# Performance work log

Hardware: AMD Instinct MI355X
Metric: run time of the kernel (lower is better)

Reference implementation:

```python
import jax, jax.numpy as jnp
import numpy as np

N_USERS = 60000
N_ITEMS = 40000
N = N_USERS + N_ITEMS   # ncount
EMB = 64
NNZ = 3200000           # nnz of sparse_norm_adj (avg degree 32)
LN_EPS = 1e-5


def setup_inputs() -> dict:
    key = jax.random.key(0)
    ks = jax.random.split(key, 12)
    ego = jax.random.normal(ks[0], (N, EMB), jnp.float32) * 0.1
    rows = jax.random.randint(ks[1], (NNZ,), 0, N)
    cols = jax.random.randint(ks[2], (NNZ,), 0, N)
    # normalized adjacency values (non-trainable buffer)
    vals = jax.random.uniform(ks[3], (NNZ,), jnp.float32) * 0.01
    # xavier-uniform-ish scale for [64,64]: sqrt(2/(64+64)) = 0.125
    w_uu = jax.random.normal(ks[4], (EMB, EMB), jnp.float32) * 0.125
    filt_uu = jax.random.uniform(ks[5], (N_USERS,), jnp.float32, 0.99, 1.01)
    par_uu = jax.random.uniform(ks[6], (2,), jnp.float32, 0.0, 0.99)
    w_ii = jax.random.normal(ks[7], (EMB, EMB), jnp.float32) * 0.125
    filt_ii = jax.random.uniform(ks[8], (N_ITEMS,), jnp.float32, 0.99, 1.01)
    par_ii = jax.random.uniform(ks[9], (2,), jnp.float32, 0.0, 0.99)
    ln_gamma = jnp.ones((EMB,), jnp.float32)
    ln_beta = jnp.zeros((EMB,), jnp.float32)
    return {"ego_embeddings": ego, "rows": rows, "cols": cols, "vals": vals,
            "w_uu": w_uu, "filt_uu": filt_uu, "par_uu": par_uu,
            "w_ii": w_ii, "filt_ii": filt_ii, "par_ii": par_ii,
            "ln_gamma": ln_gamma, "ln_beta": ln_beta}


def _spmm(rows, cols, vals, x):
    # out[rows] += vals * x[cols]  <=>  sparse_adj @ x
    return jax.ops.segment_sum(vals[:, None] * x[cols], rows, num_segments=N)


def reference(ego_embeddings, rows, cols, vals, w_uu, filt_uu, par_uu,
              w_ii, filt_ii, par_ii, ln_gamma, ln_beta):
    res = ego_embeddings
    u = ego_embeddings[:N_USERS]
    it = ego_embeddings[N_USERS:]
    # HWNN layer with K1=K2=1 collapses to par0*par1 * diag(filter) @ X @ W
    user_ego = par_uu[0] * par_uu[1] * ((filt_uu[:, None] * u) @ w_uu) + u
    item_ego = par_ii[0] * par_ii[1] * ((filt_ii[:, None] * it) @ w_ii) + it
    ego = jnp.concatenate([user_ego, item_ego], axis=0)  # [N, EMB]
    # HGCNConv (act=False): adj @ (adj.T @ ego)
    h = jax.ops.segment_sum(vals[:, None] * ego[rows], cols, num_segments=N)  # adj.T @ ego
    y = _spmm(rows, cols, vals, h)                                            # adj @ h
    # LayerNorm (eps=1e-5, affine) + residual from the ORIGINAL input
    mu = jnp.mean(y, axis=-1, keepdims=True)
    var = jnp.var(y, axis=-1, keepdims=True)
    yn = (y - mu) / jnp.sqrt(var + LN_EPS) * ln_gamma + ln_beta
    out = yn + res
    return out[:N_USERS], out[N_USERS:]
```

## Files before the change

### kernel.cpp

```cpp
#include <hip/hip_runtime.h>

#define N_USERS 60000
#define N_ITEMS 40000
#define N_TOTAL 100000
#define EMB 64
#define LN_EPS 1e-5f

#define KPS 128
#define KSH 7
#define NSUP ((N_TOTAL + KPS - 1) / KPS)
#define EPB 4096
#define BLT 512
#define TR_ROWS 32
#define XPITCH 68
#define CAP 2048
#define SPT 512

__device__ __forceinline__ float bf2f(unsigned short h)
{ return __uint_as_float(((unsigned)h) << 16); }
__device__ __forceinline__ unsigned short f2bf(float f)
{
    unsigned u = __float_as_uint(f);
    return (unsigned short)((u + 0x7FFFu + ((u >> 16) & 1u)) >> 16);
}

__global__ void transform_tile(const float* __restrict__ x,
                               const float* __restrict__ w_uu,
                               const float* __restrict__ filt_uu,
                               const float* __restrict__ par_uu,
                               const float* __restrict__ w_ii,
                               const float* __restrict__ filt_ii,
                               const float* __restrict__ par_ii,
                               unsigned short* __restrict__ out)
{
    __shared__ float Wls[EMB * EMB];
    __shared__ float xs[TR_ROWS * XPITCH];
    const int tid = threadIdx.x;
    const int r0 = blockIdx.x * TR_ROWS;
    const int itm = (r0 >= N_USERS);
    const float* W  = itm ? w_ii : w_uu;
    const float* fb = itm ? filt_ii : filt_uu;
    const int foff  = itm ? N_USERS : 0;
    const float c   = itm ? par_ii[0] * par_ii[1] : par_uu[0] * par_uu[1];

    for (int i = tid; i < EMB * EMB / 4; i += 256)
        ((float4*)Wls)[i] = ((const float4*)W)[i];
    for (int i = tid; i < TR_ROWS * 16; i += 256) {
        const float4 v = ((const float4*)x)[r0 * 16 + i];
        *(float4*)&xs[(i >> 4) * XPITCH + (i & 15) * 4] = v;
    }
    __syncthreads();

    const int lane = tid & 63;
    const int wv = tid >> 6;
    const int rg = lane >> 4;
    const int j  = lane & 15;

#pragma unroll
    for (int it = 0; it < 2; ++it) {
        const int rl = wv * 8 + it * 4 + rg;
        const int row = r0 + rl;
        float4 acc = make_float4(0.f, 0.f, 0.f, 0.f);
#pragma unroll 8
        for (int k = 0; k < EMB; ++k) {
            const float xb = xs[rl * XPITCH + k];
            const float4 w4 = *(const float4*)&Wls[k * EMB + 4 * j];
            acc.x += xb * w4.x; acc.y += xb * w4.y;
            acc.z += xb * w4.z; acc.w += xb * w4.w;
        }
        const float cf = c * fb[row - foff];
        const float4 xv = *(const float4*)&xs[rl * XPITCH + 4 * j];
        ushort4 o;
        o.x = f2bf(cf * acc.x + xv.x);
        o.y = f2bf(cf * acc.y + xv.y);
        o.z = f2bf(cf * acc.z + xv.z);
        o.w = f2bf(cf * acc.w + xv.w);
        *(ushort4*)&out[(size_t)row * EMB + 4 * j] = o;
    }
}

__global__ void hist_sup(const int* __restrict__ rows,
                         const int* __restrict__ cols,
                         int* __restrict__ cnt_r,
                         int* __restrict__ cnt_c, int nnz)
{
    __shared__ int hr[NSUP], hc[NSUP];
    const int tid = threadIdx.x;
    for (int i = tid; i < NSUP; i += 256) { hr[i] = 0; hc[i] = 0; }
    __syncthreads();
    for (int e = blockIdx.x * 256 + tid; e < nnz; e += gridDim.x * 256) {
        atomicAdd(&hr[rows[e] >> KSH], 1);
        atomicAdd(&hc[cols[e] >> KSH], 1);
    }
    __syncthreads();
    for (int i = tid; i < NSUP; i += 256) {
        if (hr[i]) atomicAdd(&cnt_r[i], hr[i]);
        if (hc[i]) atomicAdd(&cnt_c[i], hc[i]);
    }
}

__global__ void scan_sup(const int* __restrict__ cnt_c, int* __restrict__ base_c,
                         int* __restrict__ cur_c,
                         const int* __restrict__ cnt_r, int* __restrict__ base_r,
                         int* __restrict__ cur_r)
{
    const int* cnt = blockIdx.x ? cnt_r : cnt_c;
    int* base = blockIdx.x ? base_r : base_c;
    int* cur  = blockIdx.x ? cur_r  : cur_c;
    __shared__ int wsum[16];
    const int i = threadIdx.x;
    const int lane = i & 63;
    const int wv = i >> 6;
    const int v = (i < NSUP) ? cnt[i] : 0;
    int incl = v;
#pragma unroll
    for (int off = 1; off < 64; off <<= 1) {
        const int t = __shfl_up(incl, off, 64);
        if (lane >= off) incl += t;
    }
    if (lane == 63) wsum[wv] = incl;
    __syncthreads();
    if (i == 0) {
        int run = 0;
#pragma unroll
        for (int w = 0; w < 16; ++w) { const int t = wsum[w]; wsum[w] = run; run += t; }
        base[NSUP] = run;
    }
    __syncthreads();
    const int excl = wsum[wv] + incl - v;
    if (i < NSUP) { base[i] = excl; cur[i] = excl; }
}

__global__ void __launch_bounds__(BLT, 3)
build_both(const int* __restrict__ rows,
           const int* __restrict__ cols,
           const float* __restrict__ vals,
           int* __restrict__ cur_c, int2* __restrict__ pairs_c,
           int* __restrict__ cur_r, int2* __restrict__ pairs_r, int nnz)
{
    __shared__ int2 stage[EPB];
    __shared__ unsigned short sg[EPB];
    __shared__ int hist_c[NSUP];
    __shared__ int hist_r[NSUP];
    __shared__ int gbase[NSUP];
    __shared__ int lcur[NSUP];
    __shared__ int wsum[8];

    const int tid = threadIdx.x;
    const int e0 = blockIdx.x * EPB;
    const int ecnt = min(EPB, nnz - e0);

    for (int i = tid; i < NSUP; i += BLT) { hist_c[i] = 0; hist_r[i] = 0; }
    __syncthreads();

    int myr[EPB / BLT], myc[EPB / BLT];
    float myv[EPB / BLT];
#pragma unroll
    for (int i = 0; i < EPB / BLT; ++i) {
        const int s = tid + i * BLT;
        if (s < ecnt) {
            const int e = e0 + s;
            myr[i] = rows[e]; myc[i] = cols[e]; myv[i] = vals[e];
            atomicAdd(&hist_c[myc[i] >> KSH], 1);
            atomicAdd(&hist_r[myr[i] >> KSH], 1);
        } else myr[i] = -1;
    }
    __syncthreads();

#pragma unroll 1
    for (int p = 0; p < 2; ++p) {
        int* hist = p ? hist_r : hist_c;
        int* gcur = p ? cur_r  : cur_c;
        int2* out = p ? pairs_r : pairs_c;

        {
            const int lane = tid & 63;
            const int wv = tid >> 6;
            const int i0 = tid * 2;
            const int va = (i0     < NSUP) ? hist[i0]     : 0;
            const int vb = (i0 + 1 < NSUP) ? hist[i0 + 1] : 0;
            const int tsum = va + vb;
            int incl = tsum;
#pragma unroll
            for (int off = 1; off < 64; off <<= 1) {
                const int t = __shfl_up(incl, off, 64);
                if (lane >= off) incl += t;
            }
            if (lane == 63) wsum[wv] = incl;
            __syncthreads();
            int woff = 0;
            for (int w = 0; w < wv; ++w) woff += wsum[w];
            const int excl = woff + incl - tsum;
            if (i0 < NSUP) {
                lcur[i0] = excl;
                gbase[i0] = va ? atomicAdd(&gcur[i0], va) : 0;
                hist[i0] = excl;
            }
            if (i0 + 1 < NSUP) {
                lcur[i0 + 1] = excl + va;
                gbase[i0 + 1] = vb ? atomicAdd(&gcur[i0 + 1], vb) : 0;
                hist[i0 + 1] = excl + va;
            }
        }
        __syncthreads();

#pragma unroll
        for (int i = 0; i < EPB / BLT; ++i) {
            if (myr[i] >= 0) {
                const int key   = p ? myr[i] : myc[i];
                const int other = p ? myc[i] : myr[i];
                const int g = key >> KSH;
                const int s = atomicAdd(&lcur[g], 1);
                stage[s] = make_int2(other | ((key & (KPS - 1)) << 20),
                                     __float_as_int(myv[i]));
                sg[s] = (unsigned short)g;
            }
        }
        __syncthreads();

        for (int s = tid; s < ecnt; s += BLT) {
            const int g = sg[s];
            out[gbase[g] + (s - hist[g])] = stage[s];
        }
        __syncthreads();
    }
}

template <bool LN>
__global__ void __launch_bounds__(SPT, 6)
spmm_fused(const int* __restrict__ base,
           const int2* __restrict__ pairs,
           const unsigned short* __restrict__ src,
           const float* __restrict__ ego,
           const float* __restrict__ gamma,
           const float* __restrict__ beta,
           unsigned short* __restrict__ dstb,
           float* __restrict__ dstf)
{
    __shared__ int2 stage[CAP];
    __shared__ int2 sorted[CAP];
    __shared__ int cnt[KPS];
    __shared__ int kbase[KPS];
    __shared__ int kcur[KPS];

    const int tid = threadIdx.x;
    const int sup = blockIdx.x;
    const int beg = base[sup];
    const int end = base[sup + 1];
    const int g = tid >> 4;
    const int l = tid & 15;

    float4 acc[4];
#pragma unroll
    for (int i = 0; i < 4; ++i) acc[i] = make_float4(0.f, 0.f, 0.f, 0.f);

    if (tid < KPS) cnt[tid] = 0;
    __syncthreads();

    int c0 = beg;
    int csz = min(CAP, end - c0);
    for (int i = tid; i < csz; i += SPT) {
        const int2 v = pairs[c0 + i];
        stage[i] = v;
        atomicAdd(&cnt[(v.x >> 20) & (KPS - 1)], 1);
    }
    __syncthreads();

    while (csz > 0) {
        if (tid < 64) {
            const int ca = cnt[tid * 2];
            const int cb = cnt[tid * 2 + 1];
            const int tsum = ca + cb;
            int incl = tsum;
#pragma unroll
            for (int off = 1; off < 64; off <<= 1) {
                const int t = __shfl_up(incl, off, 64);
                if (tid >= off) incl += t;
            }
            const int run = incl - tsum;
            kbase[tid * 2] = run;          kcur[tid * 2] = run;
            kbase[tid * 2 + 1] = run + ca; kcur[tid * 2 + 1] = run + ca;
            cnt[tid * 2] = 0; cnt[tid * 2 + 1] = 0;
        }
        __syncthreads();

        for (int i = tid; i < csz; i += SPT) {
            const int2 v = stage[i];
            const int pos = atomicAdd(&kcur[(v.x >> 20) & (KPS - 1)], 1);
            sorted[pos] = v;
        }
        __syncthreads();

        const int nc0 = c0 + csz;
        const int ncsz = min(CAP, end - nc0);

#pragma unroll
        for (int rr = 0; rr < 4; ++rr) {
            const int k = g * 4 + rr;
            int j = kbase[k];
            const int e = kcur[k];
            float4 a = acc[rr];
            for (; j + 8 <= e; j += 8) {
                int2 p[8]; ushort4 s[8];
#pragma unroll
                for (int u = 0; u < 8; ++u) p[u] = sorted[j + u];
#pragma unroll
                for (int u = 0; u < 8; ++u)
                    s[u] = ((const ushort4*)(src + (size_t)(p[u].x & 0x1FFFF) * EMB))[l];
#pragma unroll
                for (int u = 0; u < 8; ++u) {
                    const float v = __int_as_float(p[u].y);
                    a.x += v * bf2f(s[u].x); a.y += v * bf2f(s[u].y);
                    a.z += v * bf2f(s[u].z); a.w += v * bf2f(s[u].w);
                }
            }
            for (; j + 4 <= e; j += 4) {
                int2 p[4]; ushort4 s[4];
#pragma unroll
                for (int u = 0; u < 4; ++u) p[u] = sorted[j + u];
#pragma unroll
                for (int u = 0; u < 4; ++u)
                    s[u] = ((const ushort4*)(src + (size_t)(p[u].x & 0x1FFFF) * EMB))[l];
#pragma unroll
                for (int u = 0; u < 4; ++u) {
                    const float v = __int_as_float(p[u].y);
                    a.x += v * bf2f(s[u].x); a.y += v * bf2f(s[u].y);
                    a.z += v * bf2f(s[u].z); a.w += v * bf2f(s[u].w);
                }
            }
            for (; j < e; ++j) {
                const int2 p = sorted[j];
                const ushort4 s = ((const ushort4*)(src + (size_t)(p.x & 0x1FFFF) * EMB))[l];
                const float v = __int_as_float(p.y);
                a.x += v * bf2f(s.x); a.y += v * bf2f(s.y);
                a.z += v * bf2f(s.z); a.w += v * bf2f(s.w);
            }
            acc[rr] = a;
        }

        for (int i = tid; i < ncsz; i += SPT) {
            const int2 v = pairs[nc0 + i];
            stage[i] = v;
            atomicAdd(&cnt[(v.x >> 20) & (KPS - 1)], 1);
        }
        c0 = nc0; csz = ncsz;
        __syncthreads();
    }

    const int r0 = sup * KPS + g * 4;
    if (!LN) {
#pragma unroll
        for (int rr = 0; rr < 4; ++rr) {
            const int row = r0 + rr;
            if (row < N_TOTAL) {
                ushort4 o;
                o.x = f2bf(acc[rr].x); o.y = f2bf(acc[rr].y);
                o.z = f2bf(acc[rr].z); o.w = f2bf(acc[rr].w);
                ((ushort4*)dstb)[(size_t)row * 16 + l] = o;
            }
        }
    } else {
        const float4 gm = ((const float4*)gamma)[l];
        const float4 bt = ((const float4*)beta)[l];
#pragma unroll
        for (int rr = 0; rr < 4; ++rr) {
            const int row = r0 + rr;
            const float4 a = acc[rr];
            float s  = a.x + a.y + a.z + a.w;
            float s2 = a.x * a.x + a.y * a.y + a.z * a.z + a.w * a.w;
#pragma unroll
            for (int m = 1; m <= 8; m <<= 1) {
                s  += __shfl_xor(s,  m, 64);
                s2 += __shfl_xor(s2, m, 64);
            }
            const float mu  = s * (1.0f / EMB);
            const float var = s2 * (1.0f / EMB) - mu * mu;
            const float inv = rsqrtf(var + LN_EPS);
            if (row < N_TOTAL) {
                const float4 eg = ((const float4*)(ego + (size_t)row * EMB))[l];
                float4 o;
                o.x = (a.x - mu) * inv * gm.x + bt.x + eg.x;
                o.y = (a.y - mu) * inv * gm.y + bt.y + eg.y;
                o.z = (a.z - mu) * inv * gm.z + bt.z + eg.z;
                o.w = (a.w - mu) * inv * gm.w + bt.w + eg.w;
                ((float4*)(dstf + (size_t)row * EMB))[l] = o;
            }
        }
    }
}

__global__ void transform_kernel(const float* __restrict__ x,
                                 const float* __restrict__ W,
                                 const float* __restrict__ filt,
                                 const float* __restrict__ par,
                                 float* __restrict__ out, int nrows)
{
    __shared__ float Ws[EMB * EMB];
    const int tid = threadIdx.x;
    for (int i = tid; i < EMB * EMB; i += blockDim.x) Ws[i] = W[i];
    __syncthreads();
    const float c = par[0] * par[1];
    const int lane = tid & 63;
    const int wave = tid >> 6;
    const int r0 = blockIdx.x * 32;
    for (int rr = wave; rr < 32; rr += 4) {
        const int r = r0 + rr;
        if (r >= nrows) break;
        const float xv = x[(size_t)r * EMB + lane];
        float acc = 0.f;
#pragma unroll
        for (int k = 0; k < EMB; ++k) {
            const float xk = __shfl(xv, k, 64);
            acc += xk * Ws[k * EMB + lane];
        }
        out[(size_t)r * EMB + lane] = c * filt[r] * acc + xv;
    }
}

__global__ void spmm_scatter(const int* __restrict__ src_idx,
                             const int* __restrict__ dst_idx,
                             const float* __restrict__ vals,
                             const float* __restrict__ src,
                             float* __restrict__ dst, int nnz)
{
    const long long t = (long long)blockIdx.x * blockDim.x + threadIdx.x;
    const int e = (int)(t >> 4);
    const int l = (int)(t & 15);
    if (e >= nnz) return;
    const int s = src_idx[e];
    const int d = dst_idx[e];
    const float v = vals[e];
    const float4 xv = ((const float4*)(src + (size_t)s * EMB))[l];
    float* dp = dst + (size_t)d * EMB + l * 4;
    atomicAdd(dp + 0, v * xv.x);
    atomicAdd(dp + 1, v * xv.y);
    atomicAdd(dp + 2, v * xv.z);
    atomicAdd(dp + 3, v * xv.w);
}

__global__ void ln_residual(const float* y,
                            const float* __restrict__ ego,
                            const float* __restrict__ gamma,
                            const float* __restrict__ beta,
                            float* out, int nrows)
{
    const int lane = threadIdx.x & 63;
    const int wave = threadIdx.x >> 6;
    const int r = blockIdx.x * 4 + wave;
    if (r >= nrows) return;
    const float v = y[(size_t)r * EMB + lane];
    float s = v, s2 = v * v;
#pragma unroll
    for (int off = 32; off > 0; off >>= 1) {
        s  += __shfl_down(s,  off, 64);
        s2 += __shfl_down(s2, off, 64);
    }
    s  = __shfl(s,  0, 64);
    s2 = __shfl(s2, 0, 64);
    const float mu  = s * (1.0f / EMB);
    const float var = s2 * (1.0f / EMB) - mu * mu;
    const float inv = rsqrtf(var + LN_EPS);
    out[(size_t)r * EMB + lane] =
        (v - mu) * inv * gamma[lane] + beta[lane] + ego[(size_t)r * EMB + lane];
}

extern "C" void kernel_launch(void* const* d_in, const int* in_sizes, int n_in,
                              void* d_out, int out_size, void* d_ws, size_t ws_size,
                              hipStream_t stream)
{
    const float* ego     = (const float*)d_in[0];
    const int*   rows    = (const int*)  d_in[1];
    const int*   cols    = (const int*)  d_in[2];
    const float* vals    = (const float*)d_in[3];
    const float* w_uu    = (const float*)d_in[4];
    const float* filt_uu = (const float*)d_in[5];
    const float* par_uu  = (const float*)d_in[6];
    const float* w_ii    = (const float*)d_in[7];
    const float* filt_ii = (const float*)d_in[8];
    const float* par_ii  = (const float*)d_in[9];
    const float* gamma   = (const float*)d_in[10];
    const float* beta    = (const float*)d_in[11];
    float* out = (float*)d_out;
    const int nnz = in_sizes[1];

    const size_t emb_elems = (size_t)N_TOTAL * EMB;
    const size_t emb_bytes = emb_elems * sizeof(float);
    const size_t bf_bytes  = emb_elems * sizeof(unsigned short);

    const size_t need = 2 * bf_bytes + 2 * (size_t)nnz * sizeof(int2)
                        + (size_t)(6 * (NSUP + 1)) * sizeof(int);

    if (ws_size >= need) {
        unsigned short* ego2b = (unsigned short*)d_ws;
        unsigned short* hb    = ego2b + emb_elems;
        int2* pairs_c = (int2*)(hb + emb_elems);
        int2* pairs_r = pairs_c + nnz;
        int*  cnt_c  = (int*)(pairs_r + nnz);
        int*  cnt_r  = cnt_c + NSUP;
        int*  base_c = cnt_r + NSUP;
        int*  cur_c  = base_c + (NSUP + 1);
        int*  base_r = cur_c + NSUP;
        int*  cur_r  = base_r + (NSUP + 1);

        hipMemsetAsync(cnt_c, 0, 2 * NSUP * sizeof(int), stream);

        hist_sup<<<512, 256, 0, stream>>>(rows, cols, cnt_r, cnt_c, nnz);
        scan_sup<<<2, 1024, 0, stream>>>(cnt_c, base_c, cur_c,
                                         cnt_r, base_r, cur_r);

        transform_tile<<<N_TOTAL / TR_ROWS, 256, 0, stream>>>(
            ego, w_uu, filt_uu, par_uu, w_ii, filt_ii, par_ii, ego2b);

        const int l1b = (nnz + EPB - 1) / EPB;
        build_both<<<l1b, BLT, 0, stream>>>(rows, cols, vals,
                                            cur_c, pairs_c, cur_r, pairs_r, nnz);

        spmm_fused<false><<<NSUP, SPT, 0, stream>>>(
            base_c, pairs_c, ego2b, nullptr, nullptr, nullptr, hb, nullptr);

        spmm_fused<true><<<NSUP, SPT, 0, stream>>>(
            base_r, pairs_r, hb, ego, gamma, beta, nullptr, out);
    } else {
        float* ego2 = (float*)d_ws;
        float* h    = ego2 + emb_elems;
        hipMemsetAsync(h,   0, emb_bytes, stream);
        hipMemsetAsync(out, 0, emb_bytes, stream);

        transform_kernel<<<(N_USERS + 31) / 32, 256, 0, stream>>>(
            ego, w_uu, filt_uu, par_uu, ego2, N_USERS);
        transform_kernel<<<(N_ITEMS + 31) / 32, 256, 0, stream>>>(
            ego + (size_t)N_USERS * EMB, w_ii, filt_ii, par_ii,
            ego2 + (size_t)N_USERS * EMB, N_ITEMS);

        const long long thr = (long long)nnz * 16;
        const int sblocks = (int)((thr + 255) / 256);
        spmm_scatter<<<sblocks, 256, 0, stream>>>(rows, cols, vals, ego2, h, nnz);
        spmm_scatter<<<sblocks, 256, 0, stream>>>(cols, rows, vals, h, out, nnz);

        const int rb = (N_TOTAL + 3) / 4;
        ln_residual<<<rb, 256, 0, stream>>>(out, ego, gamma, beta, out, N_TOTAL);
    }
}
```

Baseline: 405.8 us.

## Vectorize histogram loads, halve build block size, precompute scatter offsets

The histogram kernel now reads rows and cols four at a time with int4 loads, with a scalar tail for leftover elements. The build kernel handles 2048 edges per block instead of 4096 and raises its launch-bounds occupancy hint from 3 to 8. It also folds the global base minus local offset into a single per-bucket value, so the scatter loop does one shared lookup per element. Smaller blocks mean more blocks, and so more global atomics on the bucket cursors plus shorter contiguous write runs per bucket. The higher occupancy target may also force register limits.

```diff
diff --git a/kernel.cpp b/kernel.cpp
--- a/kernel.cpp
+++ b/kernel.cpp
@@ -9,8 +9,9 @@
 #define KPS 128
 #define KSH 7
 #define NSUP ((N_TOTAL + KPS - 1) / KPS)
-#define EPB 4096
+#define EPB 2048
 #define BLT 512
+#define EPT (EPB / BLT)
 #define TR_ROWS 32
 #define XPITCH 68
 #define CAP 2048
@@ -88,7 +89,16 @@
     const int tid = threadIdx.x;
     for (int i = tid; i < NSUP; i += 256) { hr[i] = 0; hc[i] = 0; }
     __syncthreads();
-    for (int e = blockIdx.x * 256 + tid; e < nnz; e += gridDim.x * 256) {
+    const int nq = nnz >> 2;
+    for (int q = blockIdx.x * 256 + tid; q < nq; q += gridDim.x * 256) {
+        const int4 r4 = ((const int4*)rows)[q];
+        const int4 c4 = ((const int4*)cols)[q];
+        atomicAdd(&hr[r4.x >> KSH], 1); atomicAdd(&hc[c4.x >> KSH], 1);
+        atomicAdd(&hr[r4.y >> KSH], 1); atomicAdd(&hc[c4.y >> KSH], 1);
+        atomicAdd(&hr[r4.z >> KSH], 1); atomicAdd(&hc[c4.z >> KSH], 1);
+        atomicAdd(&hr[r4.w >> KSH], 1); atomicAdd(&hc[c4.w >> KSH], 1);
+    }
+    for (int e = (nq << 2) + blockIdx.x * 256 + tid; e < nnz; e += gridDim.x * 256) {
         atomicAdd(&hr[rows[e] >> KSH], 1);
         atomicAdd(&hc[cols[e] >> KSH], 1);
     }
@@ -131,7 +141,7 @@
     if (i < NSUP) { base[i] = excl; cur[i] = excl; }
 }
 
-__global__ void __launch_bounds__(BLT, 3)
+__global__ void __launch_bounds__(BLT, 8)
 build_both(const int* __restrict__ rows,
            const int* __restrict__ cols,
            const float* __restrict__ vals,
@@ -142,7 +152,7 @@
     __shared__ unsigned short sg[EPB];
     __shared__ int hist_c[NSUP];
     __shared__ int hist_r[NSUP];
-    __shared__ int gbase[NSUP];
+    __shared__ int goff[NSUP];
     __shared__ int lcur[NSUP];
     __shared__ int wsum[8];
 
@@ -153,10 +163,10 @@
     for (int i = tid; i < NSUP; i += BLT) { hist_c[i] = 0; hist_r[i] = 0; }
     __syncthreads();
 
-    int myr[EPB / BLT], myc[EPB / BLT];
-    float myv[EPB / BLT];
-#pragma unroll
-    for (int i = 0; i < EPB / BLT; ++i) {
+    int myr[EPT], myc[EPT];
+    float myv[EPT];
+#pragma unroll
+    for (int i = 0; i < EPT; ++i) {
         const int s = tid + i * BLT;
         if (s < ecnt) {
             const int e = e0 + s;
@@ -169,7 +179,7 @@
 
 #pragma unroll 1
     for (int p = 0; p < 2; ++p) {
-        int* hist = p ? hist_r : hist_c;
+        const int* hist = p ? hist_r : hist_c;
         int* gcur = p ? cur_r  : cur_c;
         int2* out = p ? pairs_r : pairs_c;
 
@@ -192,20 +202,20 @@
             for (int w = 0; w < wv; ++w) woff += wsum[w];
             const int excl = woff + incl - tsum;
             if (i0 < NSUP) {
+                const int gb = va ? atomicAdd(&gcur[i0], va) : 0;
                 lcur[i0] = excl;
-                gbase[i0] = va ? atomicAdd(&gcur[i0], va) : 0;
-                hist[i0] = excl;
+                goff[i0] = gb - excl;
             }
             if (i0 + 1 < NSUP) {
+                const int gb = vb ? atomicAdd(&gcur[i0 + 1], vb) : 0;
                 lcur[i0 + 1] = excl + va;
-                gbase[i0 + 1] = vb ? atomicAdd(&gcur[i0 + 1], vb) : 0;
-                hist[i0 + 1] = excl + va;
+                goff[i0 + 1] = gb - (excl + va);
             }
         }
         __syncthreads();
 
 #pragma unroll
-        for (int i = 0; i < EPB / BLT; ++i) {
+        for (int i = 0; i < EPT; ++i) {
             if (myr[i] >= 0) {
                 const int key   = p ? myr[i] : myc[i];
                 const int other = p ? myc[i] : myr[i];
@@ -218,10 +228,8 @@
         }
         __syncthreads();
 
-        for (int s = tid; s < ecnt; s += BLT) {
-            const int g = sg[s];
-            out[gbase[g] + (s - hist[g])] = stage[s];
-        }
+        for (int s = tid; s < ecnt; s += BLT)
+            out[goff[sg[s]] + s] = stage[s];
         __syncthreads();
     }
 }
```

After: 453.0 us. 1.12x slower.
